# Kernel optimization log

Hardware: AMD Instinct MI355X
Metric: run time of the kernel (lower is better)

## Reference

```python
import jax, jax.numpy as jnp
import numpy as np

DIM = 1024
NUM_HEADS = 16
HEAD_DIM = DIM // NUM_HEADS
MLP_HIDDEN = 4 * DIM
TAU = 2.0
EPS = 1e-6
ALPHA_INIT = 0.01


def _xavier(key, out_f, in_f):
    limit = float(np.sqrt(6.0 / (in_f + out_f)))
    return jax.random.uniform(key, (out_f, in_f), jnp.float32, -limit, limit)


def setup_inputs() -> dict:
    key = jax.random.key(0)
    ks = jax.random.split(key, 10)
    B, Lq, Lkv = 4, 512, 2048
    return {
        "q_tokens": jax.random.normal(ks[0], (B, Lq, DIM), jnp.float32),
        "kv_tokens": jax.random.normal(ks[1], (B, Lkv, DIM), jnp.float32),
        "q_ln_w": jnp.ones((DIM,), jnp.float32),
        "q_ln_b": jnp.zeros((DIM,), jnp.float32),
        "kv_ln_w": jnp.ones((DIM,), jnp.float32),
        "kv_ln_b": jnp.zeros((DIM,), jnp.float32),
        "mlp_ln_w": jnp.ones((DIM,), jnp.float32),
        "mlp_ln_b": jnp.zeros((DIM,), jnp.float32),
        "Wq": _xavier(ks[2], DIM, DIM),
        "Wk": _xavier(ks[3], DIM, DIM),
        "Wv": _xavier(ks[4], DIM, DIM),
        "Wo": _xavier(ks[5], DIM, DIM),
        "bo": jnp.zeros((DIM,), jnp.float32),
        "fc1_w": _xavier(ks[6], MLP_HIDDEN, DIM),
        "fc1_b": jnp.zeros((MLP_HIDDEN,), jnp.float32),
        "fc2_w": _xavier(ks[7], DIM, MLP_HIDDEN),
        "fc2_b": jnp.zeros((DIM,), jnp.float32),
        "alpha_attn": jnp.full((1,), ALPHA_INIT, jnp.float32),
        "alpha_mlp": jnp.full((1,), ALPHA_INIT, jnp.float32),
    }


def _ln(x, w, b):
    mu = jnp.mean(x, axis=-1, keepdims=True)
    var = jnp.var(x, axis=-1, keepdims=True)
    return (x - mu) * jax.lax.rsqrt(var + EPS) * w + b


def _l2norm(x):
    # matches torch F.normalize: x / max(||x||, eps)
    n = jnp.sqrt(jnp.sum(x * x, axis=-1, keepdims=True))
    return x / jnp.maximum(n, EPS)


def reference(q_tokens, kv_tokens, q_ln_w, q_ln_b, kv_ln_w, kv_ln_b,
              mlp_ln_w, mlp_ln_b, Wq, Wk, Wv, Wo, bo,
              fc1_w, fc1_b, fc2_w, fc2_b, alpha_attn, alpha_mlp):
    B, Lq, D = q_tokens.shape
    q = _ln(q_tokens, q_ln_w, q_ln_b) @ Wq.T  # [B,Lq,D]
    kvn = _ln(kv_tokens, kv_ln_w, kv_ln_b)
    k = kvn @ Wk.T
    v = kvn @ Wv.T
    # split heads -> [B,H,L,hd]
    q = q.reshape(B, Lq, NUM_HEADS, HEAD_DIM)
    k = k.reshape(B, -1, NUM_HEADS, HEAD_DIM)
    v = v.reshape(B, -1, NUM_HEADS, HEAD_DIM)
    q = _l2norm(q)
    k = _l2norm(k)
    scores = jnp.einsum('bqhd,bkhd->bhqk', q, k) / TAU
    attn = jax.nn.softmax(scores, axis=-1)
    ctx = jnp.einsum('bhqk,bkhd->bqhd', attn, v).reshape(B, Lq, D)
    ctx = ctx @ Wo.T + bo
    out = q_tokens + alpha_attn * ctx
    h = _ln(out, mlp_ln_w, mlp_ln_b)
    h = jax.nn.gelu(h @ fc1_w.T + fc1_b, approximate=False)
    h = h @ fc2_w.T + fc2_b
    return out + alpha_mlp * h
```

## Files before the change

### kernel.cpp

```cpp
#include <hip/hip_runtime.h>


typedef __attribute__((ext_vector_type(8))) short short8_t;
typedef __attribute__((ext_vector_type(4))) short short4_t;
typedef __attribute__((ext_vector_type(4))) float f32x4_t;

#define WSCALE 16.0f
#define OSC (1.0f / 16.0f)

__device__ __forceinline__ float b2f(short s) {
    union { float f; unsigned u; } c;
    c.u = ((unsigned)(unsigned short)s) << 16;
    return c.f;
}
__device__ __forceinline__ short f2b(float f) {
    union { float f; unsigned u; } c;
    c.f = f;
    unsigned u = c.u;
    unsigned r = (u + 0x7FFFu + ((u >> 16) & 1u)) >> 16;
    return (short)r;
}
__device__ __forceinline__ unsigned cvt_pk_bf16(float lo, float hi) {
    unsigned r;
    asm("v_cvt_pk_bf16_f32 %0, %1, %2" : "=v"(r) : "v"(lo), "v"(hi));
    return r;
}
__device__ __forceinline__ unsigned f2f8_pk4(float a, float b, float c, float d) {
    int lo = __builtin_amdgcn_cvt_pk_fp8_f32(a, b, 0, false);
    return (unsigned)__builtin_amdgcn_cvt_pk_fp8_f32(c, d, lo, true);
}
__device__ __forceinline__ unsigned char f2f8(float a) {
    return (unsigned char)(__builtin_amdgcn_cvt_pk_fp8_f32(a, a, 0, false) & 0xff);
}

__device__ __forceinline__ void gload16(const void* g, void* l) {
    __builtin_amdgcn_global_load_lds(
        (const __attribute__((address_space(1))) void*)g,
        (__attribute__((address_space(3))) void*)l, 16, 0, 0);
}

template <int OUT8>
__device__ __forceinline__ void ln_row(
    const float* __restrict__ x, const float* __restrict__ w,
    const float* __restrict__ bia, void* __restrict__ y,
    int row, int tid, float* red)
{
    const float4 t = *(const float4*)(x + (size_t)row * 1024 + tid * 4);
    float v[4] = {t.x, t.y, t.z, t.w};
    float s = v[0] + v[1] + v[2] + v[3];
    float s2 = v[0]*v[0] + v[1]*v[1] + v[2]*v[2] + v[3]*v[3];
    #pragma unroll
    for (int off = 1; off < 64; off <<= 1) {
        s  += __shfl_xor(s, off);
        s2 += __shfl_xor(s2, off);
    }
    const int wave = tid >> 6, lane = tid & 63;
    if (lane == 0) { red[wave] = s; red[4 + wave] = s2; }
    __syncthreads();
    s  = red[0] + red[1] + red[2] + red[3];
    s2 = red[4] + red[5] + red[6] + red[7];
    const float mu  = s * (1.0f / 1024.0f);
    const float var = s2 * (1.0f / 1024.0f) - mu * mu;
    const float rstd = rsqrtf(var + 1e-6f);
    const float4 wv = *(const float4*)(w + tid * 4);
    const float4 bv = *(const float4*)(bia + tid * 4);
    const float o0 = (v[0] - mu) * rstd * wv.x + bv.x;
    const float o1 = (v[1] - mu) * rstd * wv.y + bv.y;
    const float o2 = (v[2] - mu) * rstd * wv.z + bv.z;
    const float o3 = (v[3] - mu) * rstd * wv.w + bv.w;
    if (OUT8) {
        ((unsigned*)y)[(size_t)row * 256 + tid] = f2f8_pk4(o0, o1, o2, o3);
    } else {
        short4 o;
        o.x = f2b(o0); o.y = f2b(o1); o.z = f2b(o2); o.w = f2b(o3);
        *(short4*)((short*)y + (size_t)row * 1024 + tid * 4) = o;
    }
}

__global__ __launch_bounds__(256) void prep_kernel(
    const float* __restrict__ qt, const float* __restrict__ kvt,
    const float* __restrict__ qlw, const float* __restrict__ qlb,
    const float* __restrict__ klw, const float* __restrict__ klb,
    short* __restrict__ qn, unsigned char* __restrict__ kvn8,
    const float* __restrict__ Wq, const float* __restrict__ Wo,
    const float* __restrict__ Wk, const float* __restrict__ Wv,
    const float* __restrict__ fc1w, const float* __restrict__ fc2w,
    short* __restrict__ Wq_b, short* __restrict__ Wo_b,
    unsigned char* __restrict__ Wkv8,
    unsigned char* __restrict__ fc1_8, unsigned char* __restrict__ fc2_8)
{
    __shared__ float red[8];
    const int bid = blockIdx.x, tid = threadIdx.x;
    if (bid < 2048) {
        ln_row<0>(qt, qlw, qlb, qn, bid, tid, red);
    } else if (bid < 10240) {
        ln_row<1>(kvt, klw, klb, kvn8, bid - 2048, tid, red);
    } else {
        int f = (bid - 10240) * 256 + tid;
        if (f < 524288) {
            const float* src = (f < 262144) ? Wq : Wo;
            short* dst = (f < 262144) ? Wq_b : Wo_b;
            const int off = f & 262143;
            const float4 v = ((const float4*)src)[off];
            short4 o;
            o.x = f2b(v.x); o.y = f2b(v.y); o.z = f2b(v.z); o.w = f2b(v.w);
            ((short4*)dst)[off] = o;
        } else {
            const float* src; unsigned* dst; int off;
            if (f < 1048576) {
                off = f - 524288;
                src = (off < 262144) ? Wk : Wv;
                dst = (unsigned*)Wkv8;
                if (off >= 262144) { src = Wv; }
                const int so = (off < 262144) ? off : off - 262144;
                const float4 v = ((const float4*)src)[so];
                dst[off] = f2f8_pk4(v.x * WSCALE, v.y * WSCALE,
                                    v.z * WSCALE, v.w * WSCALE);
                return;
            } else if (f < 2097152) {
                off = f - 1048576; src = fc1w; dst = (unsigned*)fc1_8;
            } else {
                off = f - 2097152; src = fc2w; dst = (unsigned*)fc2_8;
            }
            const float4 v = ((const float4*)src)[off];
            dst[off] = f2f8_pk4(v.x * WSCALE, v.y * WSCALE,
                                v.z * WSCALE, v.w * WSCALE);
        }
    }
}

__global__ __launch_bounds__(256) void ln8_kernel(
    const float* __restrict__ x, const float* __restrict__ w,
    const float* __restrict__ bia, unsigned char* __restrict__ y)
{
    __shared__ float red[8];
    ln_row<1>(x, w, bia, y, blockIdx.x, threadIdx.x, red);
}

template <int EPI, int BM>
__global__ __launch_bounds__(256) void gemm_bt_kernel(
    const short* __restrict__ A, const short* __restrict__ W,
    int M, int N, int Ks, int Kst,
    const float* __restrict__ bias,
    const float* __restrict__ resF,
    const float* __restrict__ alpha,
    short* __restrict__ out16,
    float* __restrict__ outF)
{
    constexpr int MI = (BM + 31) / 32;
    __shared__ __attribute__((aligned(16))) short As[2][BM * 64];
    __shared__ __attribute__((aligned(16))) short Bs[2][128 * 64];
    const int bm = blockIdx.y * BM, bn = blockIdx.x * 128;
    const int tid = threadIdx.x;
    const int wave = tid >> 6, lane = tid & 63;
    const int wm = (wave >> 1) * (BM / 2), wn = (wave & 1) * 64;
    const int l15 = lane & 15, quad = lane >> 4;
    const int l7 = l15 & 7;

    f32x4_t acc[MI][4];
    #pragma unroll
    for (int mi = 0; mi < MI; ++mi)
        #pragma unroll
        for (int ni = 0; ni < 4; ++ni)
            acc[mi][ni] = (f32x4_t){0.f, 0.f, 0.f, 0.f};

    auto stage = [&](int buf, int k0) {
        #pragma unroll
        for (int c = 0; c < BM / 32; ++c) {
            const int o = c * 4096 + tid * 16;
            const int row = o >> 7;
            const int g = ((o >> 4) & 7) ^ (row & 7);
            gload16(A + (size_t)(bm + row) * Kst + k0 + g * 8,
                    (char*)As[buf] + c * 4096 + wave * 1024);
        }
        #pragma unroll
        for (int c = 0; c < 4; ++c) {
            const int o = c * 4096 + tid * 16;
            const int row = o >> 7;
            const int g = ((o >> 4) & 7) ^ (row & 7);
            gload16(W + (size_t)(bn + row) * Kst + k0 + g * 8,
                    (char*)Bs[buf] + c * 4096 + wave * 1024);
        }
    };

    const int nIter = Ks >> 6;
    stage(0, 0);
    for (int it = 0; it < nIter; ++it) {
        const int buf = it & 1;
        __syncthreads();
        if (it + 1 < nIter) stage(buf ^ 1, (it + 1) * 64);
        #pragma unroll
        for (int h = 0; h < 2; ++h) {
            const int fg = (((h << 2) | quad) ^ l7) * 8;
            short8_t af[MI], bf[4];
            #pragma unroll
            for (int mi = 0; mi < MI; ++mi)
                af[mi] = *(const short8_t*)&As[buf][(wm + mi * 16 + l15) * 64 + fg];
            #pragma unroll
            for (int ni = 0; ni < 4; ++ni)
                bf[ni] = *(const short8_t*)&Bs[buf][(wn + ni * 16 + l15) * 64 + fg];
            #pragma unroll
            for (int mi = 0; mi < MI; ++mi)
                #pragma unroll
                for (int ni = 0; ni < 4; ++ni)
                    acc[mi][ni] = __builtin_amdgcn_mfma_f32_16x16x32_bf16(
                        af[mi], bf[ni], acc[mi][ni], 0, 0, 0);
        }
    }

    if (EPI == 4) {
        #pragma unroll
        for (int mi = 0; mi < MI; ++mi)
            #pragma unroll
            for (int r = 0; r < 4; ++r) {
                float s = 0.f;
                #pragma unroll
                for (int ni = 0; ni < 4; ++ni) {
                    const float x = acc[mi][ni][r];
                    s += x * x;
                }
                s += __shfl_xor(s, 1); s += __shfl_xor(s, 2);
                s += __shfl_xor(s, 4); s += __shfl_xor(s, 8);
                const float sc = 1.0f / fmaxf(sqrtf(s), 1e-6f);
                #pragma unroll
                for (int ni = 0; ni < 4; ++ni) acc[mi][ni][r] *= sc;
            }
    }

    const float a = (EPI == 1) ? alpha[0] : 0.f;
    #pragma unroll
    for (int mi = 0; mi < MI; ++mi) {
        #pragma unroll
        for (int ni = 0; ni < 4; ++ni) {
            const int n = bn + wn + ni * 16 + l15;
            const float bb = (EPI == 1) ? bias[n] : 0.f;
            #pragma unroll
            for (int r = 0; r < 4; ++r) {
                const int m = bm + wm + mi * 16 + (quad << 2) + r;
                const float x = acc[mi][ni][r];
                if (EPI == 4) {
                    out16[(size_t)m * N + n] = f2b(x);
                } else {
                    const size_t idx = (size_t)m * N + n;
                    outF[idx] = resF[idx] + a * (x + bb);
                }
            }
        }
    }
}

template <int EPI, int BM, int BK>
__global__ __launch_bounds__(256, 4) void gemm_f8_kernel(
    const unsigned char* __restrict__ A, const unsigned char* __restrict__ W,
    int M, int N, int Ks, int Kst,
    const float* __restrict__ bias,
    unsigned char* __restrict__ out8,
    short* __restrict__ out16,
    float* __restrict__ outF)
{
    constexpr int MI = BM / 32;
    constexpr int KS = BK / 32;
    constexpr int STG = 2 * BM * BK + 2 * 128 * BK;
    constexpr int EPIB = (EPI == 8) ? 128 * 136 * 2 : ((EPI == 2) ? BM * 144 : 0);
    constexpr int POOL = (STG > EPIB) ? STG : EPIB;
    __shared__ __attribute__((aligned(16))) unsigned char pool[POOL];
    auto AsBuf = [&](int b) { return pool + b * (BM * BK); };
    auto BsBuf = [&](int b) { return pool + 2 * BM * BK + b * (128 * BK); };
    const int bm = blockIdx.y * BM, bn = blockIdx.x * 128;
    const size_t kbase = (size_t)blockIdx.z * Ks;
    const int tid = threadIdx.x;
    const int wave = tid >> 6, lane = tid & 63;
    const int wm = (wave >> 1) * (BM / 2), wn = (wave & 1) * 64;
    const int l15 = lane & 15, quad = lane >> 4;
    const int l7 = l15 & 7;

    f32x4_t acc[MI][4];
    #pragma unroll
    for (int mi = 0; mi < MI; ++mi)
        #pragma unroll
        for (int ni = 0; ni < 4; ++ni)
            acc[mi][ni] = (f32x4_t){0.f, 0.f, 0.f, 0.f};

    auto stage = [&](int buf, int k0) {
        #pragma unroll
        for (int c = 0; c < BM * BK / 4096; ++c) {
            const int o = c * 4096 + tid * 16;
            const int row = o / BK;
            int g;
            if constexpr (BK == 128) g = ((o >> 4) & 7) ^ (row & 7);
            else                     g = ((o >> 4) & 3) ^ ((row >> 1) & 3);
            gload16(A + (size_t)(bm + row) * Kst + kbase + k0 + g * 16,
                    (char*)AsBuf(buf) + c * 4096 + wave * 1024);
        }
        #pragma unroll
        for (int c = 0; c < 128 * BK / 4096; ++c) {
            const int o = c * 4096 + tid * 16;
            const int row = o / BK;
            int g;
            if constexpr (BK == 128) g = ((o >> 4) & 7) ^ (row & 7);
            else                     g = ((o >> 4) & 3) ^ ((row >> 1) & 3);
            gload16(W + (size_t)(bn + row) * Kst + kbase + k0 + g * 16,
                    (char*)BsBuf(buf) + c * 4096 + wave * 1024);
        }
    };

    const int nIter = Ks / BK;
    stage(0, 0);
    for (int it = 0; it < nIter; ++it) {
        const int buf = it & 1;
        __syncthreads();
        if (it + 1 < nIter) stage(buf ^ 1, (it + 1) * BK);
        #pragma unroll
        for (int ks = 0; ks < KS; ++ks) {
            int fo;
            if constexpr (BK == 128)
                fo = ((((ks << 1) | (quad >> 1)) ^ l7) << 4) + (quad & 1) * 8;
            else
                fo = ((((ks << 1) | (quad >> 1)) ^ ((l15 >> 1) & 3)) << 4) +
                     (quad & 1) * 8;
            long af[MI], bf[4];
            #pragma unroll
            for (int mi = 0; mi < MI; ++mi)
                af[mi] = *(const long*)(AsBuf(buf) + (wm + mi * 16 + l15) * BK + fo);
            #pragma unroll
            for (int ni = 0; ni < 4; ++ni)
                bf[ni] = *(const long*)(BsBuf(buf) + (wn + ni * 16 + l15) * BK + fo);
            #pragma unroll
            for (int mi = 0; mi < MI; ++mi)
                #pragma unroll
                for (int ni = 0; ni < 4; ++ni)
                    acc[mi][ni] = __builtin_amdgcn_mfma_f32_16x16x32_fp8_fp8(
                        af[mi], bf[ni], acc[mi][ni], 0, 0, 0);
        }
    }

    if (EPI == 8) {
        const bool isK = (bn < 1024);
        if (isK) {
            #pragma unroll
            for (int mi = 0; mi < MI; ++mi)
                #pragma unroll
                for (int r = 0; r < 4; ++r) {
                    float s = 0.f;
                    #pragma unroll
                    for (int ni = 0; ni < 4; ++ni) {
                        const float x = acc[mi][ni][r];
                        s += x * x;
                    }
                    s += __shfl_xor(s, 1); s += __shfl_xor(s, 2);
                    s += __shfl_xor(s, 4); s += __shfl_xor(s, 8);
                    const float sc = 1.0f / fmaxf(sqrtf(s), 1e-6f);
                    #pragma unroll
                    for (int ni = 0; ni < 4; ++ni) acc[mi][ni][r] *= sc;
                }
        }
        __syncthreads();
        short* Ct = (short*)pool;
        constexpr int LDC = 136;
        if (isK) {
            #pragma unroll
            for (int mi = 0; mi < MI; ++mi)
                #pragma unroll
                for (int ni = 0; ni < 4; ++ni) {
                    const int n = wn + ni * 16 + l15;
                    #pragma unroll
                    for (int r = 0; r < 4; ++r)
                        Ct[(wm + mi * 16 + (quad << 2) + r) * LDC + n] =
                            f2b(acc[mi][ni][r]);
                }
        } else {
            #pragma unroll
            for (int mi = 0; mi < MI; ++mi)
                #pragma unroll
                for (int ni = 0; ni < 4; ++ni) {
                    short4 pk;
                    pk.x = f2b(acc[mi][ni][0] * OSC);
                    pk.y = f2b(acc[mi][ni][1] * OSC);
                    pk.z = f2b(acc[mi][ni][2] * OSC);
                    pk.w = f2b(acc[mi][ni][3] * OSC);
                    *(short4*)&Ct[(wn + ni * 16 + l15) * LDC +
                                  wm + mi * 16 + (quad << 2)] = pk;
                }
        }
        __syncthreads();
        const int b_ = bm >> 11;
        const int kv0 = bm & 2047;
        #pragma unroll
        for (int p = 0; p < 8; ++p) {
            const int idx = p * 256 + tid;
            const int row = idx >> 4, ch = idx & 15;
            const short8_t v = *(const short8_t*)&Ct[row * LDC + ch * 8];
            if (isK) {
                const int hh = (bn >> 6) + (ch >> 3);
                *(short8_t*)&out16[(size_t)((b_ * 16 + hh) * 2048 + kv0 + row) * 64 +
                                   (ch & 7) * 8] = v;
            } else {
                const int nn = bn - 1024 + row;
                *(short8_t*)&((short*)outF)[(size_t)((b_ * 16 + (nn >> 6)) * 64 +
                                            (nn & 63)) * 2048 + kv0 + ch * 8] = v;
            }
        }
        return;
    }

    if (EPI == 2) {
        __syncthreads();
        unsigned char* C8 = (unsigned char*)pool;
        constexpr int LDC8 = 144;
        #pragma unroll
        for (int mi = 0; mi < MI; ++mi)
            #pragma unroll
            for (int ni = 0; ni < 4; ++ni) {
                const int n = wn + ni * 16 + l15;
                const float bb = bias[bn + n];
                #pragma unroll
                for (int r = 0; r < 4; ++r) {
                    const float t = acc[mi][ni][r] * OSC + bb;
                    C8[(wm + mi * 16 + (quad << 2) + r) * LDC8 + n] =
                        f2f8(0.5f * t * (1.0f + erff(t * 0.70710678118f)));
                }
            }
        __syncthreads();
        #pragma unroll
        for (int p = 0; p < MI; ++p) {
            const int idx = p * 256 + tid;
            const int row = idx >> 3, ch = idx & 7;
            const f32x4_t v = *(const f32x4_t*)&C8[row * LDC8 + ch * 16];
            *(f32x4_t*)&out8[(size_t)(bm + row) * N + bn + ch * 16] = v;
        }
        return;
    }

    #pragma unroll
    for (int mi = 0; mi < MI; ++mi) {
        #pragma unroll
        for (int ni = 0; ni < 4; ++ni) {
            const int n = bn + wn + ni * 16 + l15;
            #pragma unroll
            for (int r = 0; r < 4; ++r) {
                const int m = bm + wm + mi * 16 + (quad << 2) + r;
                outF[(size_t)blockIdx.z * M * N + (size_t)m * N + n] =
                    acc[mi][ni][r];
            }
        }
    }
}

__global__ __launch_bounds__(256) void reduce4_kernel(
    const float* __restrict__ parts, const float* __restrict__ resF,
    const float* __restrict__ bias, const float* __restrict__ alpha,
    float* __restrict__ out)
{
    const int i = blockIdx.x * 256 + threadIdx.x;
    const size_t MN4 = (size_t)2048 * 1024 / 4;
    const float a = alpha[0];
    const float4 b4 = ((const float4*)bias)[i & 255];
    float4 s = ((const float4*)parts)[i];
    const float4 p1 = ((const float4*)parts)[MN4 + i];
    const float4 p2 = ((const float4*)parts)[2 * MN4 + i];
    const float4 p3 = ((const float4*)parts)[3 * MN4 + i];
    const float4 rv = ((const float4*)resF)[i];
    float4 o;
    o.x = rv.x + a * ((s.x + p1.x + p2.x + p3.x) * OSC + b4.x);
    o.y = rv.y + a * ((s.y + p1.y + p2.y + p3.y) * OSC + b4.y);
    o.z = rv.z + a * ((s.z + p1.z + p2.z + p3.z) * OSC + b4.z);
    o.w = rv.w + a * ((s.w + p1.w + p2.w + p3.w) * OSC + b4.w);
    ((float4*)out)[i] = o;
}

__global__ __launch_bounds__(256, 4) void attn_kernel(
    const short* __restrict__ q, const short* __restrict__ khd,
    const short* __restrict__ vhd, float* __restrict__ o0,
    float* __restrict__ o1, float* __restrict__ lpart)
{
    const int h  = blockIdx.x;
    const int b  = blockIdx.y;
    const int qt = blockIdx.z >> 1;
    const int sp = blockIdx.z & 1;
    const int tid = threadIdx.x;
    const int wave = tid >> 6, lane = tid & 63;
    const int l15 = lane & 15, quad = lane >> 4;
    const int q0 = qt * 64 + wave * 16;
    const int t0 = sp * 16;

    __shared__ __attribute__((aligned(16))) short Ks[2][4096];
    __shared__ __attribute__((aligned(16))) short Vs[2][4096];

    const short* qbase = q + (size_t)(b * 512 + q0 + l15) * 1024 + h * 64 + quad * 8;
    const short8_t aq0 = *(const short8_t*)(qbase);
    const short8_t aq1 = *(const short8_t*)(qbase + 32);

    const short* kbase = khd + (size_t)(b * 16 + h) * 2048 * 64;
    const short* vbase = vhd + (size_t)(b * 16 + h) * 64 * 2048;

    const int swz = l15 & 7;
    const int g0 = (quad ^ swz) * 8;
    const int g1 = ((quad ^ swz) ^ 4) * 8;

    auto stage = [&](int buf, int t) {
        #pragma unroll
        for (int c = 0; c < 2; ++c) {
            const int o = c * 4096 + tid * 16;
            const int row = o >> 7;
            const int g = ((o >> 4) & 7) ^ (row & 7);
            gload16(kbase + (size_t)(t * 64 + row) * 64 + g * 8,
                    (char*)Ks[buf] + c * 4096 + wave * 1024);
            gload16(vbase + (size_t)row * 2048 + t * 64 + g * 8,
                    (char*)Vs[buf] + c * 4096 + wave * 1024);
        }
    };

    const short4_t ones4 = {(short)0x3F80, (short)0x3F80,
                            (short)0x3F80, (short)0x3F80};

    f32x4_t oacc[4];
    #pragma unroll
    for (int u = 0; u < 4; ++u) oacc[u] = (f32x4_t){0.f, 0.f, 0.f, 0.f};
    f32x4_t lacc = (f32x4_t){0.f, 0.f, 0.f, 0.f};

    stage(0, t0);
    for (int tt = 0; tt < 16; ++tt) {
        const int buf = tt & 1;
        __syncthreads();
        if (tt + 1 < 16) stage(buf ^ 1, t0 + tt + 1);

        f32x4_t s[4];
        #pragma unroll
        for (int ss = 0; ss < 4; ++ss) {
            const int R = ss * 16 + l15;
            const short8_t bk0 = *(const short8_t*)&Ks[buf][R * 64 + g0];
            const short8_t bk1 = *(const short8_t*)&Ks[buf][R * 64 + g1];
            f32x4_t a = (f32x4_t){0.f, 0.f, 0.f, 0.f};
            a = __builtin_amdgcn_mfma_f32_16x16x32_bf16(bk0, aq0, a, 0, 0, 0);
            a = __builtin_amdgcn_mfma_f32_16x16x32_bf16(bk1, aq1, a, 0, 0, 0);
            s[ss] = a;
        }
        short4_t pa[4];
        #pragma unroll
        for (int ss = 0; ss < 4; ++ss) {
            const float p0 = __expf(s[ss][0] * 0.5f);
            const float p1 = __expf(s[ss][1] * 0.5f);
            const float p2 = __expf(s[ss][2] * 0.5f);
            const float p3 = __expf(s[ss][3] * 0.5f);
            union { unsigned w[2]; short4_t v; } u_;
            u_.w[0] = cvt_pk_bf16(p0, p1);
            u_.w[1] = cvt_pk_bf16(p2, p3);
            pa[ss] = u_.v;
        }
        #pragma unroll
        for (int ss = 0; ss < 4; ++ss)
            lacc = __builtin_amdgcn_mfma_f32_16x16x16bf16_1k(
                pa[ss], ones4, lacc, 0, 0, 0);
        #pragma unroll
        for (int ss = 0; ss < 4; ++ss) {
            const int ch = (((ss * 2 + (quad >> 1)) ^ swz) << 3) + ((quad & 1) << 2);
            #pragma unroll
            for (int u = 0; u < 4; ++u) {
                const short4_t bv =
                    *(const short4_t*)&Vs[buf][(u * 16 + l15) * 64 + ch];
                oacc[u] = __builtin_amdgcn_mfma_f32_16x16x16bf16_1k(
                    pa[ss], bv, oacc[u], 0, 0, 0);
            }
        }
    }

    float* ob = sp ? o1 : o0;
    float* lb = lpart + (size_t)sp * 2048 * 16;
    #pragma unroll
    for (int u = 0; u < 4; ++u)
        #pragma unroll
        for (int r = 0; r < 4; ++r)
            ob[(size_t)(b * 512 + q0 + quad * 4 + r) * 1024 + h * 64 + u * 16 + l15] =
                oacc[u][r];
    if (l15 == 0) {
        #pragma unroll
        for (int r = 0; r < 4; ++r)
            lb[(size_t)(b * 512 + q0 + quad * 4 + r) * 16 + h] = lacc[r];
    }
}

__global__ __launch_bounds__(256) void attn_combine_kernel(
    const float* __restrict__ o0, const float* __restrict__ o1,
    const float* __restrict__ lpart, short* __restrict__ ctx)
{
    const int i = blockIdx.x * 256 + threadIdx.x;
    const int row = i >> 8;
    const int h = (i & 255) >> 4;
    const float l = lpart[row * 16 + h] + lpart[2048 * 16 + row * 16 + h];
    const float inv = 1.0f / l;
    const float4 a = ((const float4*)o0)[i];
    const float4 c = ((const float4*)o1)[i];
    short4 o;
    o.x = f2b((a.x + c.x) * inv);
    o.y = f2b((a.y + c.y) * inv);
    o.z = f2b((a.z + c.z) * inv);
    o.w = f2b((a.w + c.w) * inv);
    ((short4*)ctx)[i] = o;
}

extern "C" void kernel_launch(void* const* d_in, const int* in_sizes, int n_in,
                              void* d_out, int out_size, void* d_ws, size_t ws_size,
                              hipStream_t stream)
{
    const float* q_tokens  = (const float*)d_in[0];
    const float* kv_tokens = (const float*)d_in[1];
    const float* q_ln_w    = (const float*)d_in[2];
    const float* q_ln_b    = (const float*)d_in[3];
    const float* kv_ln_w   = (const float*)d_in[4];
    const float* kv_ln_b   = (const float*)d_in[5];
    const float* mlp_ln_w  = (const float*)d_in[6];
    const float* mlp_ln_b  = (const float*)d_in[7];
    const float* Wq        = (const float*)d_in[8];
    const float* Wk        = (const float*)d_in[9];
    const float* Wv        = (const float*)d_in[10];
    const float* Wo        = (const float*)d_in[11];
    const float* bo        = (const float*)d_in[12];
    const float* fc1_w     = (const float*)d_in[13];
    const float* fc1_b     = (const float*)d_in[14];
    const float* fc2_w     = (const float*)d_in[15];
    const float* fc2_b     = (const float*)d_in[16];
    const float* alpha_attn = (const float*)d_in[17];
    const float* alpha_mlp  = (const float*)d_in[18];

    char* ws = (char*)d_ws;
    const size_t MB = (size_t)1 << 20;
    short* khd    = (short*)(ws);
    short* vhd    = (short*)(ws + 16 * MB);
    float* parts  = (float*)(ws);
    unsigned char* kvn8 = (unsigned char*)(ws + 32 * MB);
    float* attn_o0 = (float*)(ws + 32 * MB);
    unsigned char* h1   = (unsigned char*)(ws + 32 * MB);
    short* qn     = (short*)(ws + 40 * MB);
    short* qbuf   = (short*)(ws + 44 * MB);
    short* ctx    = (short*)(ws + 48 * MB);
    float* aout   = (float*)(ws + 52 * MB);
    float* attn_o1 = (float*)(ws + 52 * MB);
    unsigned char* hn8 = (unsigned char*)(ws + 60 * MB);
    float* attn_l  = (float*)(ws + 60 * MB);
    short* Wq_b   = (short*)(ws + 62 * MB);
    short* Wo_b   = (short*)(ws + 64 * MB);
    unsigned char* Wkv8  = (unsigned char*)(ws + 66 * MB);
    unsigned char* fc1_8 = (unsigned char*)(ws + 68 * MB);
    unsigned char* fc2_8 = (unsigned char*)(ws + 72 * MB);

    prep_kernel<<<22528, 256, 0, stream>>>(
        q_tokens, kv_tokens, q_ln_w, q_ln_b, kv_ln_w, kv_ln_b, qn, kvn8,
        Wq, Wo, Wk, Wv, fc1_w, fc2_w,
        Wq_b, Wo_b, Wkv8, fc1_8, fc2_8);

    gemm_bt_kernel<4, 32><<<dim3(8, 64), 256, 0, stream>>>(
        qn, Wq_b, 2048, 1024, 1024, 1024, nullptr, nullptr, nullptr, qbuf, nullptr);
    gemm_f8_kernel<8, 128, 64><<<dim3(16, 64), 256, 0, stream>>>(
        kvn8, Wkv8, 8192, 2048, 1024, 1024, nullptr, nullptr, khd, (float*)vhd);

    attn_kernel<<<dim3(16, 4, 16), 256, 0, stream>>>(
        qbuf, khd, vhd, attn_o0, attn_o1, attn_l);
    attn_combine_kernel<<<2048, 256, 0, stream>>>(attn_o0, attn_o1, attn_l, ctx);

    gemm_bt_kernel<1, 32><<<dim3(8, 64), 256, 0, stream>>>(
        ctx, Wo_b, 2048, 1024, 1024, 1024, bo, q_tokens, alpha_attn, nullptr, aout);

    ln8_kernel<<<2048, 256, 0, stream>>>(aout, mlp_ln_w, mlp_ln_b, hn8);

    gemm_f8_kernel<2, 64, 64><<<dim3(32, 32), 256, 0, stream>>>(
        hn8, fc1_8, 2048, 4096, 1024, 1024, fc1_b, h1, nullptr, nullptr);

    gemm_f8_kernel<7, 64, 64><<<dim3(8, 32, 4), 256, 0, stream>>>(
        h1, fc2_8, 2048, 1024, 1024, 4096, nullptr, nullptr, nullptr, parts);
    reduce4_kernel<<<2048, 256, 0, stream>>>(parts, aout, fc2_b, alpha_mlp,
                                             (float*)d_out);
}
```

Baseline: 308.2 us.

## Fuse Q and KV projections into one launch; store split-K and attention partials as bf16

Merges the Q projection (bf16 GEMM) and the fused K/V projection (fp8 GEMM) into a single qkv_kernel that dispatches on blockIdx.x, removing one launch and letting both GEMMs share the GPU. Separately, the fc2 split-K partial sums and the attention split partial outputs are now written as bf16 instead of fp32, halving the bytes moved through the reduce and combine kernels. The bf16 partials lose precision before summation, and the fused kernel's shared memory pool is sized for the larger branch, which may limit occupancy for the Q-projection blocks.

```diff
diff --git a/kernel.cpp b/kernel.cpp
--- a/kernel.cpp
+++ b/kernel.cpp
@@ -249,6 +249,233 @@
     }
 }
 
+__device__ __forceinline__ void kvproj_body(
+    unsigned char* __restrict__ pool, int bx, int by, int tid,
+    const unsigned char* __restrict__ A, const unsigned char* __restrict__ W,
+    short* __restrict__ khd, short* __restrict__ vhd)
+{
+    constexpr int BM = 128, BK = 64, MI = 4, KS = 2;
+    constexpr int N = 2048, Kst = 1024;
+    auto AsBuf = [&](int b) { return pool + b * (BM * BK); };
+    auto BsBuf = [&](int b) { return pool + 2 * BM * BK + b * (128 * BK); };
+    const int bm = by * BM, bn = bx * 128;
+    const int wave = tid >> 6, lane = tid & 63;
+    const int wm = (wave >> 1) * (BM / 2), wn = (wave & 1) * 64;
+    const int l15 = lane & 15, quad = lane >> 4;
+
+    f32x4_t acc[MI][4];
+    #pragma unroll
+    for (int mi = 0; mi < MI; ++mi)
+        #pragma unroll
+        for (int ni = 0; ni < 4; ++ni)
+            acc[mi][ni] = (f32x4_t){0.f, 0.f, 0.f, 0.f};
+
+    auto stage = [&](int buf, int k0) {
+        #pragma unroll
+        for (int c = 0; c < 2; ++c) {
+            const int o = c * 4096 + tid * 16;
+            const int row = o >> 6;
+            const int g = ((o >> 4) & 3) ^ ((row >> 1) & 3);
+            gload16(A + (size_t)(bm + row) * Kst + k0 + g * 16,
+                    (char*)AsBuf(buf) + c * 4096 + wave * 1024);
+        }
+        #pragma unroll
+        for (int c = 0; c < 2; ++c) {
+            const int o = c * 4096 + tid * 16;
+            const int row = o >> 6;
+            const int g = ((o >> 4) & 3) ^ ((row >> 1) & 3);
+            gload16(W + (size_t)(bn + row) * Kst + k0 + g * 16,
+                    (char*)BsBuf(buf) + c * 4096 + wave * 1024);
+        }
+    };
+
+    stage(0, 0);
+    for (int it = 0; it < 16; ++it) {
+        const int buf = it & 1;
+        __syncthreads();
+        if (it + 1 < 16) stage(buf ^ 1, (it + 1) * BK);
+        #pragma unroll
+        for (int ks = 0; ks < KS; ++ks) {
+            const int fo = ((((ks << 1) | (quad >> 1)) ^ ((l15 >> 1) & 3)) << 4) +
+                           (quad & 1) * 8;
+            long af[MI], bf[4];
+            #pragma unroll
+            for (int mi = 0; mi < MI; ++mi)
+                af[mi] = *(const long*)(AsBuf(buf) + (wm + mi * 16 + l15) * BK + fo);
+            #pragma unroll
+            for (int ni = 0; ni < 4; ++ni)
+                bf[ni] = *(const long*)(BsBuf(buf) + (wn + ni * 16 + l15) * BK + fo);
+            #pragma unroll
+            for (int mi = 0; mi < MI; ++mi)
+                #pragma unroll
+                for (int ni = 0; ni < 4; ++ni)
+                    acc[mi][ni] = __builtin_amdgcn_mfma_f32_16x16x32_fp8_fp8(
+                        af[mi], bf[ni], acc[mi][ni], 0, 0, 0);
+        }
+    }
+
+    const bool isK = (bn < 1024);
+    if (isK) {
+        #pragma unroll
+        for (int mi = 0; mi < MI; ++mi)
+            #pragma unroll
+            for (int r = 0; r < 4; ++r) {
+                float s = 0.f;
+                #pragma unroll
+                for (int ni = 0; ni < 4; ++ni) {
+                    const float x = acc[mi][ni][r];
+                    s += x * x;
+                }
+                s += __shfl_xor(s, 1); s += __shfl_xor(s, 2);
+                s += __shfl_xor(s, 4); s += __shfl_xor(s, 8);
+                const float sc = 1.0f / fmaxf(sqrtf(s), 1e-6f);
+                #pragma unroll
+                for (int ni = 0; ni < 4; ++ni) acc[mi][ni][r] *= sc;
+            }
+    }
+    __syncthreads();
+    short* Ct = (short*)pool;
+    constexpr int LDC = 136;
+    if (isK) {
+        #pragma unroll
+        for (int mi = 0; mi < MI; ++mi)
+            #pragma unroll
+            for (int ni = 0; ni < 4; ++ni) {
+                const int n = wn + ni * 16 + l15;
+                #pragma unroll
+                for (int r = 0; r < 4; ++r)
+                    Ct[(wm + mi * 16 + (quad << 2) + r) * LDC + n] =
+                        f2b(acc[mi][ni][r]);
+            }
+    } else {
+        #pragma unroll
+        for (int mi = 0; mi < MI; ++mi)
+            #pragma unroll
+            for (int ni = 0; ni < 4; ++ni) {
+                short4 pk;
+                pk.x = f2b(acc[mi][ni][0] * OSC);
+                pk.y = f2b(acc[mi][ni][1] * OSC);
+                pk.z = f2b(acc[mi][ni][2] * OSC);
+                pk.w = f2b(acc[mi][ni][3] * OSC);
+                *(short4*)&Ct[(wn + ni * 16 + l15) * LDC +
+                              wm + mi * 16 + (quad << 2)] = pk;
+            }
+    }
+    __syncthreads();
+    const int b_ = bm >> 11;
+    const int kv0 = bm & 2047;
+    #pragma unroll
+    for (int p = 0; p < 8; ++p) {
+        const int idx = p * 256 + tid;
+        const int row = idx >> 4, ch = idx & 15;
+        const short8_t v = *(const short8_t*)&Ct[row * LDC + ch * 8];
+        if (isK) {
+            const int hh = (bn >> 6) + (ch >> 3);
+            *(short8_t*)&khd[(size_t)((b_ * 16 + hh) * 2048 + kv0 + row) * 64 +
+                             (ch & 7) * 8] = v;
+        } else {
+            const int nn = bn - 1024 + row;
+            *(short8_t*)&vhd[(size_t)((b_ * 16 + (nn >> 6)) * 64 +
+                             (nn & 63)) * 2048 + kv0 + ch * 8] = v;
+        }
+    }
+}
+
+__device__ __forceinline__ void qproj_body(
+    unsigned char* __restrict__ pool, int bx, int by, int tid,
+    const short* __restrict__ A, const short* __restrict__ W,
+    short* __restrict__ out16)
+{
+    constexpr int BM = 32, N = 1024, Kst = 1024;
+    short* As = (short*)pool;
+    short* Bs = (short*)(pool + 8192);
+    const int bm = by * BM, bn = bx * 128;
+    const int wave = tid >> 6, lane = tid & 63;
+    const int wm = (wave >> 1) * 16, wn = (wave & 1) * 64;
+    const int l15 = lane & 15, quad = lane >> 4;
+    const int l7 = l15 & 7;
+
+    f32x4_t acc[4];
+    #pragma unroll
+    for (int ni = 0; ni < 4; ++ni) acc[ni] = (f32x4_t){0.f, 0.f, 0.f, 0.f};
+
+    auto stage = [&](int buf, int k0) {
+        {
+            const int o = tid * 16;
+            const int row = o >> 7;
+            const int g = ((o >> 4) & 7) ^ (row & 7);
+            gload16(A + (size_t)(bm + row) * Kst + k0 + g * 8,
+                    (char*)As + buf * 4096 + wave * 1024);
+        }
+        #pragma unroll
+        for (int c = 0; c < 4; ++c) {
+            const int o = c * 4096 + tid * 16;
+            const int row = o >> 7;
+            const int g = ((o >> 4) & 7) ^ (row & 7);
+            gload16(W + (size_t)(bn + row) * Kst + k0 + g * 8,
+                    (char*)Bs + buf * 16384 + c * 4096 + wave * 1024);
+        }
+    };
+
+    stage(0, 0);
+    for (int it = 0; it < 16; ++it) {
+        const int buf = it & 1;
+        __syncthreads();
+        if (it + 1 < 16) stage(buf ^ 1, (it + 1) * 64);
+        #pragma unroll
+        for (int h = 0; h < 2; ++h) {
+            const int fg = (((h << 2) | quad) ^ l7) * 8;
+            const short8_t af =
+                *(const short8_t*)&As[buf * 2048 + (wm + l15) * 64 + fg];
+            short8_t bf[4];
+            #pragma unroll
+            for (int ni = 0; ni < 4; ++ni)
+                bf[ni] = *(const short8_t*)&Bs[buf * 8192 +
+                                               (wn + ni * 16 + l15) * 64 + fg];
+            #pragma unroll
+            for (int ni = 0; ni < 4; ++ni)
+                acc[ni] = __builtin_amdgcn_mfma_f32_16x16x32_bf16(
+                    af, bf[ni], acc[ni], 0, 0, 0);
+        }
+    }
+
+    #pragma unroll
+    for (int r = 0; r < 4; ++r) {
+        float s = 0.f;
+        #pragma unroll
+        for (int ni = 0; ni < 4; ++ni) {
+            const float x = acc[ni][r];
+            s += x * x;
+        }
+        s += __shfl_xor(s, 1); s += __shfl_xor(s, 2);
+        s += __shfl_xor(s, 4); s += __shfl_xor(s, 8);
+        const float sc = 1.0f / fmaxf(sqrtf(s), 1e-6f);
+        #pragma unroll
+        for (int ni = 0; ni < 4; ++ni) acc[ni][r] *= sc;
+    }
+    #pragma unroll
+    for (int ni = 0; ni < 4; ++ni) {
+        const int n = bn + wn + ni * 16 + l15;
+        #pragma unroll
+        for (int r = 0; r < 4; ++r) {
+            const int m = bm + wm + (quad << 2) + r;
+            out16[(size_t)m * N + n] = f2b(acc[ni][r]);
+        }
+    }
+}
+
+__global__ __launch_bounds__(256, 4) void qkv_kernel(
+    const unsigned char* __restrict__ kvn8, const unsigned char* __restrict__ Wkv8,
+    short* __restrict__ khd, short* __restrict__ vhd,
+    const short* __restrict__ qn, const short* __restrict__ Wq_b,
+    short* __restrict__ qbuf)
+{
+    __shared__ __attribute__((aligned(16))) unsigned char pool[40960];
+    const int bx = blockIdx.x, by = blockIdx.y, tid = threadIdx.x;
+    if (bx < 16) kvproj_body(pool, bx, by, tid, kvn8, Wkv8, khd, vhd);
+    else         qproj_body(pool, bx - 16, by, tid, qn, Wq_b, qbuf);
+}
+
 template <int EPI, int BM, int BK>
 __global__ __launch_bounds__(256, 4) void gemm_f8_kernel(
     const unsigned char* __restrict__ A, const unsigned char* __restrict__ W,
@@ -261,7 +488,7 @@
     constexpr int MI = BM / 32;
     constexpr int KS = BK / 32;
     constexpr int STG = 2 * BM * BK + 2 * 128 * BK;
-    constexpr int EPIB = (EPI == 8) ? 128 * 136 * 2 : ((EPI == 2) ? BM * 144 : 0);
+    constexpr int EPIB = (EPI == 2) ? BM * 144 : 0;
     constexpr int POOL = (STG > EPIB) ? STG : EPIB;
     __shared__ __attribute__((aligned(16))) unsigned char pool[POOL];
     auto AsBuf = [&](int b) { return pool + b * (BM * BK); };
@@ -334,75 +561,6 @@
         }
     }
 
-    if (EPI == 8) {
-        const bool isK = (bn < 1024);
-        if (isK) {
-            #pragma unroll
-            for (int mi = 0; mi < MI; ++mi)
-                #pragma unroll
-                for (int r = 0; r < 4; ++r) {
-                    float s = 0.f;
-                    #pragma unroll
-                    for (int ni = 0; ni < 4; ++ni) {
-                        const float x = acc[mi][ni][r];
-                        s += x * x;
-                    }
-                    s += __shfl_xor(s, 1); s += __shfl_xor(s, 2);
-                    s += __shfl_xor(s, 4); s += __shfl_xor(s, 8);
-                    const float sc = 1.0f / fmaxf(sqrtf(s), 1e-6f);
-                    #pragma unroll
-                    for (int ni = 0; ni < 4; ++ni) acc[mi][ni][r] *= sc;
-                }
-        }
-        __syncthreads();
-        short* Ct = (short*)pool;
-        constexpr int LDC = 136;
-        if (isK) {
-            #pragma unroll
-            for (int mi = 0; mi < MI; ++mi)
-                #pragma unroll
-                for (int ni = 0; ni < 4; ++ni) {
-                    const int n = wn + ni * 16 + l15;
-                    #pragma unroll
-                    for (int r = 0; r < 4; ++r)
-                        Ct[(wm + mi * 16 + (quad << 2) + r) * LDC + n] =
-                            f2b(acc[mi][ni][r]);
-                }
-        } else {
-            #pragma unroll
-            for (int mi = 0; mi < MI; ++mi)
-                #pragma unroll
-                for (int ni = 0; ni < 4; ++ni) {
-                    short4 pk;
-                    pk.x = f2b(acc[mi][ni][0] * OSC);
-                    pk.y = f2b(acc[mi][ni][1] * OSC);
-                    pk.z = f2b(acc[mi][ni][2] * OSC);
-                    pk.w = f2b(acc[mi][ni][3] * OSC);
-                    *(short4*)&Ct[(wn + ni * 16 + l15) * LDC +
-                                  wm + mi * 16 + (quad << 2)] = pk;
-                }
-        }
-        __syncthreads();
-        const int b_ = bm >> 11;
-        const int kv0 = bm & 2047;
-        #pragma unroll
-        for (int p = 0; p < 8; ++p) {
-            const int idx = p * 256 + tid;
-            const int row = idx >> 4, ch = idx & 15;
-            const short8_t v = *(const short8_t*)&Ct[row * LDC + ch * 8];
-            if (isK) {
-                const int hh = (bn >> 6) + (ch >> 3);
-                *(short8_t*)&out16[(size_t)((b_ * 16 + hh) * 2048 + kv0 + row) * 64 +
-                                   (ch & 7) * 8] = v;
-            } else {
-                const int nn = bn - 1024 + row;
-                *(short8_t*)&((short*)outF)[(size_t)((b_ * 16 + (nn >> 6)) * 64 +
-                                            (nn & 63)) * 2048 + kv0 + ch * 8] = v;
-            }
-        }
-        return;
-    }
-
     if (EPI == 2) {
         __syncthreads();
         unsigned char* C8 = (unsigned char*)pool;
@@ -439,15 +597,15 @@
             #pragma unroll
             for (int r = 0; r < 4; ++r) {
                 const int m = bm + wm + mi * 16 + (quad << 2) + r;
-                outF[(size_t)blockIdx.z * M * N + (size_t)m * N + n] =
-                    acc[mi][ni][r];
+                out16[(size_t)blockIdx.z * M * N + (size_t)m * N + n] =
+                    f2b(acc[mi][ni][r]);
             }
         }
     }
 }
 
 __global__ __launch_bounds__(256) void reduce4_kernel(
-    const float* __restrict__ parts, const float* __restrict__ resF,
+    const short* __restrict__ parts, const float* __restrict__ resF,
     const float* __restrict__ bias, const float* __restrict__ alpha,
     float* __restrict__ out)
 {
@@ -455,23 +613,23 @@
     const size_t MN4 = (size_t)2048 * 1024 / 4;
     const float a = alpha[0];
     const float4 b4 = ((const float4*)bias)[i & 255];
-    float4 s = ((const float4*)parts)[i];
-    const float4 p1 = ((const float4*)parts)[MN4 + i];
-    const float4 p2 = ((const float4*)parts)[2 * MN4 + i];
-    const float4 p3 = ((const float4*)parts)[3 * MN4 + i];
+    const short4 p0 = ((const short4*)parts)[i];
+    const short4 p1 = ((const short4*)parts)[MN4 + i];
+    const short4 p2 = ((const short4*)parts)[2 * MN4 + i];
+    const short4 p3 = ((const short4*)parts)[3 * MN4 + i];
     const float4 rv = ((const float4*)resF)[i];
     float4 o;
-    o.x = rv.x + a * ((s.x + p1.x + p2.x + p3.x) * OSC + b4.x);
-    o.y = rv.y + a * ((s.y + p1.y + p2.y + p3.y) * OSC + b4.y);
-    o.z = rv.z + a * ((s.z + p1.z + p2.z + p3.z) * OSC + b4.z);
-    o.w = rv.w + a * ((s.w + p1.w + p2.w + p3.w) * OSC + b4.w);
+    o.x = rv.x + a * ((b2f(p0.x) + b2f(p1.x) + b2f(p2.x) + b2f(p3.x)) * OSC + b4.x);
+    o.y = rv.y + a * ((b2f(p0.y) + b2f(p1.y) + b2f(p2.y) + b2f(p3.y)) * OSC + b4.y);
+    o.z = rv.z + a * ((b2f(p0.z) + b2f(p1.z) + b2f(p2.z) + b2f(p3.z)) * OSC + b4.z);
+    o.w = rv.w + a * ((b2f(p0.w) + b2f(p1.w) + b2f(p2.w) + b2f(p3.w)) * OSC + b4.w);
     ((float4*)out)[i] = o;
 }
 
 __global__ __launch_bounds__(256, 4) void attn_kernel(
     const short* __restrict__ q, const short* __restrict__ khd,
-    const short* __restrict__ vhd, float* __restrict__ o0,
-    float* __restrict__ o1, float* __restrict__ lpart)
+    const short* __restrict__ vhd, short* __restrict__ o0,
+    short* __restrict__ o1, float* __restrict__ lpart)
 {
     const int h  = blockIdx.x;
     const int b  = blockIdx.y;
@@ -564,14 +722,14 @@
         }
     }
 
-    float* ob = sp ? o1 : o0;
+    short* ob = sp ? o1 : o0;
     float* lb = lpart + (size_t)sp * 2048 * 16;
     #pragma unroll
     for (int u = 0; u < 4; ++u)
         #pragma unroll
         for (int r = 0; r < 4; ++r)
             ob[(size_t)(b * 512 + q0 + quad * 4 + r) * 1024 + h * 64 + u * 16 + l15] =
-                oacc[u][r];
+                f2b(oacc[u][r]);
     if (l15 == 0) {
         #pragma unroll
         for (int r = 0; r < 4; ++r)
@@ -580,7 +738,7 @@
 }
 
 __global__ __launch_bounds__(256) void attn_combine_kernel(
-    const float* __restrict__ o0, const float* __restrict__ o1,
+    const short* __restrict__ o0, const short* __restrict__ o1,
     const float* __restrict__ lpart, short* __restrict__ ctx)
 {
     const int i = blockIdx.x * 256 + threadIdx.x;
@@ -588,13 +746,13 @@
     const int h = (i & 255) >> 4;
     const float l = lpart[row * 16 + h] + lpart[2048 * 16 + row * 16 + h];
     const float inv = 1.0f / l;
-    const float4 a = ((const float4*)o0)[i];
-    const float4 c = ((const float4*)o1)[i];
+    const short4 a4 = ((const short4*)o0)[i];
+    const short4 c4 = ((const short4*)o1)[i];
     short4 o;
-    o.x = f2b((a.x + c.x) * inv);
-    o.y = f2b((a.y + c.y) * inv);
-    o.z = f2b((a.z + c.z) * inv);
-    o.w = f2b((a.w + c.w) * inv);
+    o.x = f2b((b2f(a4.x) + b2f(c4.x)) * inv);
+    o.y = f2b((b2f(a4.y) + b2f(c4.y)) * inv);
+    o.z = f2b((b2f(a4.z) + b2f(c4.z)) * inv);
+    o.w = f2b((b2f(a4.w) + b2f(c4.w)) * inv);
     ((short4*)ctx)[i] = o;
 }
 
@@ -626,15 +784,15 @@
     const size_t MB = (size_t)1 << 20;
     short* khd    = (short*)(ws);
     short* vhd    = (short*)(ws + 16 * MB);
-    float* parts  = (float*)(ws);
+    short* parts  = (short*)(ws);
     unsigned char* kvn8 = (unsigned char*)(ws + 32 * MB);
-    float* attn_o0 = (float*)(ws + 32 * MB);
+    short* attn_o0 = (short*)(ws + 32 * MB);
     unsigned char* h1   = (unsigned char*)(ws + 32 * MB);
     short* qn     = (short*)(ws + 40 * MB);
     short* qbuf   = (short*)(ws + 44 * MB);
     short* ctx    = (short*)(ws + 48 * MB);
     float* aout   = (float*)(ws + 52 * MB);
-    float* attn_o1 = (float*)(ws + 52 * MB);
+    short* attn_o1 = (short*)(ws + 52 * MB);
     unsigned char* hn8 = (unsigned char*)(ws + 60 * MB);
     float* attn_l  = (float*)(ws + 60 * MB);
     short* Wq_b   = (short*)(ws + 62 * MB);
@@ -648,10 +806,8 @@
         Wq, Wo, Wk, Wv, fc1_w, fc2_w,
         Wq_b, Wo_b, Wkv8, fc1_8, fc2_8);
 
-    gemm_bt_kernel<4, 32><<<dim3(8, 64), 256, 0, stream>>>(
-        qn, Wq_b, 2048, 1024, 1024, 1024, nullptr, nullptr, nullptr, qbuf, nullptr);
-    gemm_f8_kernel<8, 128, 64><<<dim3(16, 64), 256, 0, stream>>>(
-        kvn8, Wkv8, 8192, 2048, 1024, 1024, nullptr, nullptr, khd, (float*)vhd);
+    qkv_kernel<<<dim3(24, 64), 256, 0, stream>>>(
+        kvn8, Wkv8, khd, vhd, qn, Wq_b, qbuf);
 
     attn_kernel<<<dim3(16, 4, 16), 256, 0, stream>>>(
         qbuf, khd, vhd, attn_o0, attn_o1, attn_l);
@@ -666,7 +822,7 @@
         hn8, fc1_8, 2048, 4096, 1024, 1024, fc1_b, h1, nullptr, nullptr);
 
     gemm_f8_kernel<7, 64, 64><<<dim3(8, 32, 4), 256, 0, stream>>>(
-        h1, fc2_8, 2048, 1024, 1024, 4096, nullptr, nullptr, nullptr, parts);
+        h1, fc2_8, 2048, 1024, 1024, 4096, nullptr, nullptr, parts, nullptr);
     reduce4_kernel<<<2048, 256, 0, stream>>>(parts, aout, fc2_b, alpha_mlp,
                                              (float*)d_out);
 }
```

After: 296.0 us. 1.04x faster.
